# Kernel optimization log

Hardware: AMD Instinct MI355X
Metric: run time of the kernel (lower is better)

## Reference

```python
import jax, jax.numpy as jnp
import numpy as np

SPS_AMPLIFY = 1.5
SPS_DAMPEN = 0.3
SPS_DEEP_QUESTION = 0.1
SPS_EXCLAIM = 0.85
SPS_QUESTION = 0.25
SPS_SUPER_EXCLAIM = 0.95

B, S, D = 4, 2048, 1024
NUM_HEADS = 16
HEAD_DIM = D // NUM_HEADS
SCALE = HEAD_DIM ** (-0.5)


def sps_pro(x):
    """Piecewise elementwise modulation based on sigmoid(x) bands."""
    xn = jax.nn.sigmoid(x)
    # bands: xn>0.95 -> 2.0 ; 0.85<xn<=0.95 -> 1.5 ; xn<0.1 -> 0.1 ;
    #        0.1<=xn<0.25 -> 0.3 ; else -> 1.0
    mult = jnp.where(
        xn > SPS_SUPER_EXCLAIM, 2.0,
        jnp.where(xn > SPS_EXCLAIM, SPS_AMPLIFY,
                  jnp.where(xn < SPS_DEEP_QUESTION, 0.1,
                            jnp.where(xn < SPS_QUESTION, SPS_DAMPEN, 1.0))))
    return x * mult


def setup_inputs() -> dict:
    key = jax.random.key(0)
    k0, k1, k2, k3, k4 = jax.random.split(key, 5)
    s = 1.0 / np.sqrt(D)
    return {
        "x": jax.random.normal(k0, (B, S, D), dtype=jnp.float32),
        "W_qkv": jax.random.uniform(k1, (D, 3 * D), dtype=jnp.float32, minval=-s, maxval=s),
        "b_qkv": jax.random.uniform(k2, (3 * D,), dtype=jnp.float32, minval=-s, maxval=s),
        "W_proj": jax.random.uniform(k3, (D, D), dtype=jnp.float32, minval=-s, maxval=s),
        "b_proj": jax.random.uniform(k4, (D,), dtype=jnp.float32, minval=-s, maxval=s),
    }


def reference(x, W_qkv, b_qkv, W_proj, b_proj):
    qkv = jnp.einsum('bsd,de->bse', x, W_qkv) + b_qkv  # [B,S,3D]
    q, k, v = jnp.split(qkv, 3, axis=-1)               # each [B,S,D]
    attn = jnp.einsum('bsd,btd->bst', q, k) * SCALE    # [B,S,S]
    attn = sps_pro(attn)
    attn = jax.nn.softmax(attn, axis=-1)
    out = jnp.einsum('bst,btd->bsd', attn, v)          # [B,S,D]
    out = jnp.einsum('bsd,de->bse', out, W_proj) + b_proj
    return out
```

## Files before the change

### kernel.cpp

```cpp
#include <hip/hip_runtime.h>
#include <hip/hip_bf16.h>
#include <hip/hip_fp16.h>
#include <stdint.h>

typedef __attribute__((ext_vector_type(8))) _Float16 f16x8;
typedef __attribute__((ext_vector_type(4))) float f32x4;

__device__ __forceinline__ void async16(void* lds, const void* g) {
  __builtin_amdgcn_global_load_lds(
      (const __attribute__((address_space(1))) void*)g,
      (__attribute__((address_space(3))) void*)lds, 16, 0, 0);
}

__device__ __forceinline__ uint16_t f2h_u(float f) {
  union { __half h; uint16_t u; } c;
  c.h = __float2half(f);
  return c.u;
}

__global__ __launch_bounds__(256)
void conv_f2h(const float* __restrict__ in, uint16_t* __restrict__ out, int n4) {
  int i = blockIdx.x * 256 + threadIdx.x;
  if (i >= n4) return;
  float4 v = ((const float4*)in)[i];
  ushort4 o;
  o.x = f2h_u(v.x); o.y = f2h_u(v.y); o.z = f2h_u(v.z); o.w = f2h_u(v.w);
  ((ushort4*)out)[i] = o;
}

__global__ __launch_bounds__(256)
void trans_f2h(const float* __restrict__ in, uint16_t* __restrict__ out,
               int ldin, int ldout) {
  __shared__ float t[64][65];
  const int tx = threadIdx.x & 63, ty = threadIdx.x >> 6;
  const int r0 = blockIdx.y * 64, c0 = blockIdx.x * 64;
#pragma unroll
  for (int i = 0; i < 16; ++i)
    t[ty + i * 4][tx] = in[(size_t)(r0 + ty + i * 4) * ldin + c0 + tx];
  __syncthreads();
#pragma unroll
  for (int i = 0; i < 16; ++i)
    out[(size_t)(c0 + ty + i * 4) * ldout + r0 + tx] = f2h_u(t[tx][ty + i * 4]);
}

template <int EPI>
__global__ __launch_bounds__(512, 2)
void gemm256(const uint16_t* __restrict__ A, const uint16_t* __restrict__ B,
             void* __restrict__ Cv, void* __restrict__ Cv2,
             const float* __restrict__ bias,
             int nT, int lda, int ldb, int ldc,
             long long strA, long long strB, long long strC) {
  extern __shared__ uint16_t lds_u16[];

  const int gx = gridDim.x, gy = gridDim.y;
  const int nwg = gx * gy * gridDim.z;
  const int fid = blockIdx.x + gx * (blockIdx.y + gy * blockIdx.z);
  const int fs = (fid & 7) * (nwg >> 3) + (fid >> 3);
  const int bx = fs % gx;
  const int by = (fs / gx) % gy;
  const int bz = fs / (gx * gy);

  const int tid = threadIdx.x;
  const int l = tid & 63;
  const int w = tid >> 6;
  const int wm = w >> 1, wn = w & 1;
  const int l15 = l & 15, l4 = l >> 4;
  const int rowBase = bx * 256, colBase = by * 128;
  const uint16_t* Ag = A + (size_t)bz * strA;
  const uint16_t* Bg = B + (size_t)bz * strB;

  const uint16_t* pA[4];
  const uint16_t* pB[2];
#pragma unroll
  for (int u = 0; u < 4; ++u) {
    int c = tid + (u << 9);
    int cs = c ^ ((c >> 3) & 7);
    pA[u] = Ag + (size_t)(rowBase + (cs >> 3)) * lda + (cs & 7) * 8;
  }
#pragma unroll
  for (int u = 0; u < 2; ++u) {
    int c = tid + (u << 9);
    int cs = c ^ ((c >> 3) & 7);
    pB[u] = Bg + (size_t)(colBase + (cs >> 3)) * ldb + (cs & 7) * 8;
  }

  f32x4 acc[4][4];
#pragma unroll
  for (int m = 0; m < 4; ++m)
#pragma unroll
    for (int n = 0; n < 4; ++n)
      acc[m][n] = (f32x4){0.f, 0.f, 0.f, 0.f};

#define STAGE(t2, s2)                                                          \
  {                                                                            \
    const int kb_ = (t2) << 6;                                                 \
    uint16_t* dA_ = lds_u16 + (s2) * 24576;                                    \
    uint16_t* dB_ = dA_ + 16384;                                               \
    _Pragma("unroll") for (int u = 0; u < 4; ++u)                              \
        async16(&dA_[(size_t)(tid + (u << 9)) * 8], pA[u] + kb_);              \
    _Pragma("unroll") for (int u = 0; u < 2; ++u)                              \
        async16(&dB_[(size_t)(tid + (u << 9)) * 8], pB[u] + kb_);              \
  }

  STAGE(0, 0)
  STAGE(1, 1)
  asm volatile("s_waitcnt vmcnt(6)" ::: "memory");
  __builtin_amdgcn_s_barrier();

  int sl = 0;
  for (int t = 0; t < nT; ++t) {
    int s2 = sl + 2; if (s2 >= 3) s2 -= 3;
    if (t + 2 < nT) STAGE(t + 2, s2)
    const uint16_t* As = lds_u16 + sl * 24576;
    const uint16_t* Bs = As + 16384;
#pragma unroll
    for (int ks = 0; ks < 2; ++ks) {
      f16x8 af[4], bf[4];
#pragma unroll
      for (int m = 0; m < 4; ++m) {
        const int r = wm * 64 + m * 16 + l15;
        const int byt = r * 128 + ((ks * 64 + l4 * 16) ^ ((r & 7) << 4));
        af[m] = *(const f16x8*)((const char*)As + byt);
      }
#pragma unroll
      for (int n = 0; n < 4; ++n) {
        const int r = wn * 64 + n * 16 + l15;
        const int byt = r * 128 + ((ks * 64 + l4 * 16) ^ ((r & 7) << 4));
        bf[n] = *(const f16x8*)((const char*)Bs + byt);
      }
      __builtin_amdgcn_s_setprio(1);
#pragma unroll
      for (int m = 0; m < 4; ++m)
#pragma unroll
        for (int n = 0; n < 4; ++n)
          acc[m][n] = __builtin_amdgcn_mfma_f32_16x16x32_f16(af[m], bf[n], acc[m][n], 0, 0, 0);
      __builtin_amdgcn_s_setprio(0);
    }
    if (t + 1 < nT) {
      if (t + 2 < nT) {
        asm volatile("s_waitcnt vmcnt(6)" ::: "memory");
      } else {
        asm volatile("s_waitcnt vmcnt(0)" ::: "memory");
      }
      __builtin_amdgcn_s_barrier();
    }
    sl = (sl == 2) ? 0 : sl + 1;
  }
#undef STAGE

  const int orow0 = rowBase + wm * 64 + l4 * 4;
  const int ocol0 = colBase + wn * 64 + l15;
  if (EPI == 0) {
    uint16_t* qd = (uint16_t*)Cv;
    uint16_t* kd = (uint16_t*)Cv2;
#pragma unroll
    for (int n = 0; n < 4; ++n) {
      const int gcol = ocol0 + n * 16;
      const float bv = bias[gcol];
      uint16_t* base = (gcol < 1024 ? qd : kd) + (gcol & 1023);
#pragma unroll
      for (int m = 0; m < 4; ++m)
#pragma unroll
        for (int j = 0; j < 4; ++j) {
          const int grow = orow0 + m * 16 + j;
          base[(size_t)(grow >> 11) * 2097152 + (size_t)(grow & 2047) * 1024] =
              f2h_u(acc[m][n][j] + bv);
        }
    }
  } else if (EPI == 1) {
    uint16_t* C = (uint16_t*)Cv + (size_t)bz * strC;
#pragma unroll
    for (int n = 0; n < 4; ++n)
#pragma unroll
      for (int m = 0; m < 4; ++m)
#pragma unroll
        for (int j = 0; j < 4; ++j) {
          float xs = acc[m][n][j] * 0.125f;
          float mult = (xs > 2.94443897916644f) ? 2.0f
                     : (xs > 1.73460105538811f) ? 1.5f
                     : (xs < -2.19722457733622f) ? 0.1f
                     : (xs < -1.09861228866811f) ? 0.3f
                                                 : 1.0f;
          C[(size_t)(orow0 + m * 16 + j) * ldc + ocol0 + n * 16] = f2h_u(xs * mult);
        }
  } else if (EPI == 2) {
    uint16_t* C = (uint16_t*)Cv + (size_t)bz * strC;
#pragma unroll
    for (int m = 0; m < 4; ++m)
#pragma unroll
      for (int j = 0; j < 4; ++j) {
        const int d = orow0 + m * 16 + j;
        const float bv = bias[d];
#pragma unroll
        for (int n = 0; n < 4; ++n)
          C[(size_t)d * ldc + ocol0 + n * 16] = f2h_u(acc[m][n][j] + bv);
      }
  } else if (EPI == 3) {
    uint16_t* C = (uint16_t*)Cv + (size_t)bz * strC;
#pragma unroll
    for (int n = 0; n < 4; ++n)
#pragma unroll
      for (int m = 0; m < 4; ++m)
#pragma unroll
        for (int j = 0; j < 4; ++j)
          C[(size_t)(orow0 + m * 16 + j) * ldc + ocol0 + n * 16] = f2h_u(acc[m][n][j]);
  } else {
    float* C = (float*)Cv;
#pragma unroll
    for (int n = 0; n < 4; ++n) {
      const float bv = bias[ocol0 + n * 16];
#pragma unroll
      for (int m = 0; m < 4; ++m)
#pragma unroll
        for (int j = 0; j < 4; ++j)
          C[(size_t)(orow0 + m * 16 + j) * ldc + ocol0 + n * 16] = acc[m][n][j] + bv;
    }
  }
}

__global__ __launch_bounds__(256)
void softmax_rows(uint16_t* __restrict__ P) {
  const size_t row = blockIdx.x;
  uint16_t* p = P + row * 2048;
  const int tid = threadIdx.x;
  uint4 raw = *(const uint4*)(p + tid * 8);
  uint32_t w[4] = {raw.x, raw.y, raw.z, raw.w};
  float v[8];
#pragma unroll
  for (int q = 0; q < 4; ++q) {
    __half2 h = *(__half2*)&w[q];
    float2 f = __half22float2(h);
    v[2 * q] = f.x;
    v[2 * q + 1] = f.y;
  }
  float mx = v[0];
#pragma unroll
  for (int j = 1; j < 8; ++j) mx = fmaxf(mx, v[j]);
#pragma unroll
  for (int o = 32; o > 0; o >>= 1) mx = fmaxf(mx, __shfl_xor(mx, o));
  __shared__ float redm[4], reds[4];
  if ((tid & 63) == 0) redm[tid >> 6] = mx;
  __syncthreads();
  mx = fmaxf(fmaxf(redm[0], redm[1]), fmaxf(redm[2], redm[3]));
  float e[8];
  float se = 0.f;
#pragma unroll
  for (int j = 0; j < 8; ++j) { e[j] = __expf(v[j] - mx); se += e[j]; }
#pragma unroll
  for (int o = 32; o > 0; o >>= 1) se += __shfl_xor(se, o);
  if ((tid & 63) == 0) reds[tid >> 6] = se;
  __syncthreads();
  se = (reds[0] + reds[1]) + (reds[2] + reds[3]);
  const float inv = 1.0f / se;
  uint32_t wo[4];
#pragma unroll
  for (int q = 0; q < 4; ++q) {
    uint16_t a = f2h_u(e[2 * q] * inv);
    uint16_t b = f2h_u(e[2 * q + 1] * inv);
    wo[q] = (uint32_t)a | ((uint32_t)b << 16);
  }
  uint4 ov;
  ov.x = wo[0]; ov.y = wo[1]; ov.z = wo[2]; ov.w = wo[3];
  *(uint4*)(p + tid * 8) = ov;
}

extern "C" void kernel_launch(void* const* d_in, const int* in_sizes, int n_in,
                              void* d_out, int out_size, void* d_ws, size_t ws_size,
                              hipStream_t stream) {
  const float* x     = (const float*)d_in[0];
  const float* Wqkv  = (const float*)d_in[1];
  const float* bqkv  = (const float*)d_in[2];
  const float* Wproj = (const float*)d_in[3];
  const float* bproj = (const float*)d_in[4];
  float* out = (float*)d_out;

  char* ws = (char*)d_ws;
  size_t off = 0;
  auto alloc = [&](size_t bytes) -> void* {
    void* p = ws + off;
    off += (bytes + 255) & ~(size_t)255;
    return p;
  };
  uint16_t* xh    = (uint16_t*)alloc(8192ULL * 1024 * 2);
  uint16_t* WqkT  = (uint16_t*)alloc(2048ULL * 1024 * 2);
  uint16_t* WvT   = (uint16_t*)alloc(1024ULL * 1024 * 2);
  uint16_t* WpT   = (uint16_t*)alloc(1024ULL * 1024 * 2);
  uint16_t* qh    = (uint16_t*)alloc(4ULL * 2048 * 1024 * 2);
  uint16_t* kh    = (uint16_t*)alloc(4ULL * 2048 * 1024 * 2);
  uint16_t* vT    = (uint16_t*)alloc(4ULL * 1024 * 2048 * 2);
  uint16_t* Pm    = (uint16_t*)alloc(4ULL * 2048 * 2048 * 2);
  uint16_t* ao    = xh;

  conv_f2h<<<8192, 256, 0, stream>>>(x, xh, 2097152);
  trans_f2h<<<dim3(32, 16), 256, 0, stream>>>(Wqkv, WqkT, 3072, 1024);
  trans_f2h<<<dim3(16, 16), 256, 0, stream>>>(Wqkv + 2048, WvT, 3072, 1024);
  trans_f2h<<<dim3(16, 16), 256, 0, stream>>>(Wproj, WpT, 1024, 1024);
  gemm256<0><<<dim3(32, 16, 1), 512, 147456, stream>>>(
      xh, WqkT, qh, kh, bqkv, 16, 1024, 1024, 0, 0, 0, 0);
  gemm256<2><<<dim3(4, 16, 4), 512, 147456, stream>>>(
      WvT, xh, vT, nullptr, bqkv + 2048, 16, 1024, 1024, 2048,
      0, 2097152LL, 2097152LL);
  gemm256<1><<<dim3(8, 16, 4), 512, 147456, stream>>>(
      qh, kh, Pm, nullptr, nullptr, 16, 1024, 1024, 2048,
      2097152LL, 2097152LL, 4194304LL);
  softmax_rows<<<8192, 256, 0, stream>>>(Pm);
  gemm256<3><<<dim3(8, 8, 4), 512, 147456, stream>>>(
      Pm, vT, ao, nullptr, nullptr, 32, 2048, 2048, 1024,
      4194304LL, 2097152LL, 2097152LL);
  gemm256<4><<<dim3(32, 8, 1), 512, 147456, stream>>>(
      ao, WpT, out, nullptr, bproj, 16, 1024, 1024, 1024, 0, 0, 0);
}
```

Baseline: 229.9 us.

## Fuse V projection into QK GEMM and split async staging across k-substeps

Merges the separate V-projection GEMM into the Q/K projection GEMM by transposing the full W_qkv at once and extending the grid to 3072 output columns. The epilogue writes the V columns transposed, packing four contiguous rows per store. It also splits the next-tile async LDS loads into two halves issued inside each k-substep, with extra barriers between substeps. This removes one kernel launch and one transpose launch, and improves load overlap with MFMA work, at the cost of more barriers per tile and uncoalesced-ish transposed V stores.

```diff
diff --git a/kernel.cpp b/kernel.cpp
--- a/kernel.cpp
+++ b/kernel.cpp
@@ -46,7 +46,7 @@
 template <int EPI>
 __global__ __launch_bounds__(512, 2)
 void gemm256(const uint16_t* __restrict__ A, const uint16_t* __restrict__ B,
-             void* __restrict__ Cv, void* __restrict__ Cv2,
+             void* __restrict__ Cv, void* __restrict__ Cv2, void* __restrict__ Cv3,
              const float* __restrict__ bias,
              int nT, int lda, int ldb, int ldc,
              long long strA, long long strB, long long strC) {
@@ -91,26 +91,24 @@
     for (int n = 0; n < 4; ++n)
       acc[m][n] = (f32x4){0.f, 0.f, 0.f, 0.f};
 
-#define STAGE(t2, s2)                                                          \
+#define STAGE_H(t2, s2, h)                                                     \
   {                                                                            \
     const int kb_ = (t2) << 6;                                                 \
     uint16_t* dA_ = lds_u16 + (s2) * 24576;                                    \
     uint16_t* dB_ = dA_ + 16384;                                               \
-    _Pragma("unroll") for (int u = 0; u < 4; ++u)                              \
-        async16(&dA_[(size_t)(tid + (u << 9)) * 8], pA[u] + kb_);              \
-    _Pragma("unroll") for (int u = 0; u < 2; ++u)                              \
-        async16(&dB_[(size_t)(tid + (u << 9)) * 8], pB[u] + kb_);              \
-  }
-
-  STAGE(0, 0)
-  STAGE(1, 1)
+    async16(&dA_[(size_t)(tid + ((2 * (h)) << 9)) * 8], pA[2 * (h)] + kb_);    \
+    async16(&dA_[(size_t)(tid + ((2 * (h) + 1) << 9)) * 8], pA[2 * (h) + 1] + kb_); \
+    async16(&dB_[(size_t)(tid + ((h) << 9)) * 8], pB[h] + kb_);                \
+  }
+
+  STAGE_H(0, 0, 0) STAGE_H(0, 0, 1)
+  STAGE_H(1, 1, 0) STAGE_H(1, 1, 1)
   asm volatile("s_waitcnt vmcnt(6)" ::: "memory");
   __builtin_amdgcn_s_barrier();
 
   int sl = 0;
   for (int t = 0; t < nT; ++t) {
     int s2 = sl + 2; if (s2 >= 3) s2 -= 3;
-    if (t + 2 < nT) STAGE(t + 2, s2)
     const uint16_t* As = lds_u16 + sl * 24576;
     const uint16_t* Bs = As + 16384;
 #pragma unroll
@@ -128,6 +126,8 @@
         const int byt = r * 128 + ((ks * 64 + l4 * 16) ^ ((r & 7) << 4));
         bf[n] = *(const f16x8*)((const char*)Bs + byt);
       }
+      if (t + 2 < nT) STAGE_H(t + 2, s2, ks)
+      __builtin_amdgcn_s_barrier();
       __builtin_amdgcn_s_setprio(1);
 #pragma unroll
       for (int m = 0; m < 4; ++m)
@@ -135,37 +135,55 @@
         for (int n = 0; n < 4; ++n)
           acc[m][n] = __builtin_amdgcn_mfma_f32_16x16x32_f16(af[m], bf[n], acc[m][n], 0, 0, 0);
       __builtin_amdgcn_s_setprio(0);
-    }
-    if (t + 1 < nT) {
-      if (t + 2 < nT) {
-        asm volatile("s_waitcnt vmcnt(6)" ::: "memory");
-      } else {
-        asm volatile("s_waitcnt vmcnt(0)" ::: "memory");
+      if (ks == 0) {
+        __builtin_amdgcn_s_barrier();
+      } else if (t + 1 < nT) {
+        if (t + 2 < nT) {
+          asm volatile("s_waitcnt vmcnt(6)" ::: "memory");
+        } else {
+          asm volatile("s_waitcnt vmcnt(0)" ::: "memory");
+        }
+        __builtin_amdgcn_s_barrier();
       }
-      __builtin_amdgcn_s_barrier();
     }
     sl = (sl == 2) ? 0 : sl + 1;
   }
-#undef STAGE
+#undef STAGE_H
 
   const int orow0 = rowBase + wm * 64 + l4 * 4;
   const int ocol0 = colBase + wn * 64 + l15;
   if (EPI == 0) {
     uint16_t* qd = (uint16_t*)Cv;
     uint16_t* kd = (uint16_t*)Cv2;
+    uint16_t* vt = (uint16_t*)Cv3;
 #pragma unroll
     for (int n = 0; n < 4; ++n) {
       const int gcol = ocol0 + n * 16;
       const float bv = bias[gcol];
-      uint16_t* base = (gcol < 1024 ? qd : kd) + (gcol & 1023);
-#pragma unroll
-      for (int m = 0; m < 4; ++m)
-#pragma unroll
-        for (int j = 0; j < 4; ++j) {
-          const int grow = orow0 + m * 16 + j;
-          base[(size_t)(grow >> 11) * 2097152 + (size_t)(grow & 2047) * 1024] =
-              f2h_u(acc[m][n][j] + bv);
+      if (gcol < 2048) {
+        uint16_t* base = (gcol < 1024 ? qd : kd) + (gcol & 1023);
+#pragma unroll
+        for (int m = 0; m < 4; ++m)
+#pragma unroll
+          for (int j = 0; j < 4; ++j) {
+            const int grow = orow0 + m * 16 + j;
+            base[(size_t)(grow >> 11) * 2097152 + (size_t)(grow & 2047) * 1024] =
+                f2h_u(acc[m][n][j] + bv);
+          }
+      } else {
+        const int d = gcol - 2048;
+#pragma unroll
+        for (int m = 0; m < 4; ++m) {
+          const int grow0 = orow0 + m * 16;
+          ushort4 o;
+          o.x = f2h_u(acc[m][n][0] + bv);
+          o.y = f2h_u(acc[m][n][1] + bv);
+          o.z = f2h_u(acc[m][n][2] + bv);
+          o.w = f2h_u(acc[m][n][3] + bv);
+          *(ushort4*)&vt[(size_t)(grow0 >> 11) * 2097152 + (size_t)d * 2048 +
+                         (grow0 & 2047)] = o;
         }
+      }
     }
   } else if (EPI == 1) {
     uint16_t* C = (uint16_t*)Cv + (size_t)bz * strC;
@@ -183,18 +201,6 @@
                                                  : 1.0f;
           C[(size_t)(orow0 + m * 16 + j) * ldc + ocol0 + n * 16] = f2h_u(xs * mult);
         }
-  } else if (EPI == 2) {
-    uint16_t* C = (uint16_t*)Cv + (size_t)bz * strC;
-#pragma unroll
-    for (int m = 0; m < 4; ++m)
-#pragma unroll
-      for (int j = 0; j < 4; ++j) {
-        const int d = orow0 + m * 16 + j;
-        const float bv = bias[d];
-#pragma unroll
-        for (int n = 0; n < 4; ++n)
-          C[(size_t)d * ldc + ocol0 + n * 16] = f2h_u(acc[m][n][j] + bv);
-      }
   } else if (EPI == 3) {
     uint16_t* C = (uint16_t*)Cv + (size_t)bz * strC;
 #pragma unroll
@@ -282,8 +288,7 @@
     return p;
   };
   uint16_t* xh    = (uint16_t*)alloc(8192ULL * 1024 * 2);
-  uint16_t* WqkT  = (uint16_t*)alloc(2048ULL * 1024 * 2);
-  uint16_t* WvT   = (uint16_t*)alloc(1024ULL * 1024 * 2);
+  uint16_t* WqkvT = (uint16_t*)alloc(3072ULL * 1024 * 2);
   uint16_t* WpT   = (uint16_t*)alloc(1024ULL * 1024 * 2);
   uint16_t* qh    = (uint16_t*)alloc(4ULL * 2048 * 1024 * 2);
   uint16_t* kh    = (uint16_t*)alloc(4ULL * 2048 * 1024 * 2);
@@ -292,21 +297,17 @@
   uint16_t* ao    = xh;
 
   conv_f2h<<<8192, 256, 0, stream>>>(x, xh, 2097152);
-  trans_f2h<<<dim3(32, 16), 256, 0, stream>>>(Wqkv, WqkT, 3072, 1024);
-  trans_f2h<<<dim3(16, 16), 256, 0, stream>>>(Wqkv + 2048, WvT, 3072, 1024);
+  trans_f2h<<<dim3(48, 16), 256, 0, stream>>>(Wqkv, WqkvT, 3072, 1024);
   trans_f2h<<<dim3(16, 16), 256, 0, stream>>>(Wproj, WpT, 1024, 1024);
-  gemm256<0><<<dim3(32, 16, 1), 512, 147456, stream>>>(
-      xh, WqkT, qh, kh, bqkv, 16, 1024, 1024, 0, 0, 0, 0);
-  gemm256<2><<<dim3(4, 16, 4), 512, 147456, stream>>>(
-      WvT, xh, vT, nullptr, bqkv + 2048, 16, 1024, 1024, 2048,
-      0, 2097152LL, 2097152LL);
+  gemm256<0><<<dim3(32, 24, 1), 512, 147456, stream>>>(
+      xh, WqkvT, qh, kh, vT, bqkv, 16, 1024, 1024, 0, 0, 0, 0);
   gemm256<1><<<dim3(8, 16, 4), 512, 147456, stream>>>(
-      qh, kh, Pm, nullptr, nullptr, 16, 1024, 1024, 2048,
+      qh, kh, Pm, nullptr, nullptr, nullptr, 16, 1024, 1024, 2048,
       2097152LL, 2097152LL, 4194304LL);
   softmax_rows<<<8192, 256, 0, stream>>>(Pm);
   gemm256<3><<<dim3(8, 8, 4), 512, 147456, stream>>>(
-      Pm, vT, ao, nullptr, nullptr, 32, 2048, 2048, 1024,
+      Pm, vT, ao, nullptr, nullptr, nullptr, 32, 2048, 2048, 1024,
       4194304LL, 2097152LL, 2097152LL);
   gemm256<4><<<dim3(32, 8, 1), 512, 147456, stream>>>(
-      ao, WpT, out, nullptr, bproj, 16, 1024, 1024, 1024, 0, 0, 0);
-}
+      ao, WpT, out, nullptr, nullptr, bproj, 16, 1024, 1024, 1024, 0, 0, 0);
+}
```

After: 235.4 us. +2.4%, slower.
